# Kernel optimization log

Measured on AMD Instinct MI355X. Metric: run time of the kernel, lower is better.

## Reference

```python
import jax, jax.numpy as jnp
import numpy as np

B, S, D_MODEL, H = 4, 2048, 2048, 16
HD = D_MODEL // H  # 128
ROPE_BASE = 10000.0


def apply_rope(x):
    # x: [B, H, S, HD]; interleaved-pair rotary embedding along seq axis
    s, d = x.shape[2], x.shape[3]
    inv_freq = 1.0 / (ROPE_BASE ** (jnp.arange(0, d, 2, dtype=jnp.float32) / d))  # [d/2]
    ang = jnp.arange(s, dtype=jnp.float32)[:, None] * inv_freq[None, :]  # [S, d/2]
    cos, sin = jnp.cos(ang), jnp.sin(ang)
    x0, x1 = x[..., 0::2], x[..., 1::2]  # [B,H,S,d/2]
    o0 = x0 * cos - x1 * sin
    o1 = x0 * sin + x1 * cos
    return jnp.stack([o0, o1], axis=-1).reshape(x.shape)


def setup_inputs() -> dict:
    key = jax.random.key(0)
    ks = jax.random.split(key, 5)
    sc = 1.0 / np.sqrt(D_MODEL)
    return {
        "x": jax.random.normal(ks[0], (B, S, D_MODEL), dtype=jnp.float32),
        "Wq": jax.random.normal(ks[1], (D_MODEL, D_MODEL), dtype=jnp.float32) * sc,
        "Wk": jax.random.normal(ks[2], (D_MODEL, D_MODEL), dtype=jnp.float32) * sc,
        "Wv": jax.random.normal(ks[3], (D_MODEL, D_MODEL), dtype=jnp.float32) * sc,
        "Wo": jax.random.normal(ks[4], (D_MODEL, D_MODEL), dtype=jnp.float32) * sc,
        "bo": jnp.zeros((D_MODEL,), dtype=jnp.float32),
    }


def reference(x, Wq, Wk, Wv, Wo, bo):
    b, s, _ = x.shape
    # torch Linear: y = x @ W.T (no qkv bias)
    q = (x @ Wq.T).reshape(b, s, H, HD).transpose(0, 2, 1, 3)  # [B,H,S,HD]
    k = (x @ Wk.T).reshape(b, s, H, HD).transpose(0, 2, 1, 3)
    v = (x @ Wv.T).reshape(b, s, H, HD).transpose(0, 2, 1, 3)
    q = apply_rope(q)
    k = apply_rope(k)
    scores = jnp.einsum("bhqd,bhkd->bhqk", q, k)
    causal = jnp.tril(jnp.ones((s, s), dtype=bool))
    scores = jnp.where(causal, scores, -jnp.inf)
    attn = jax.nn.softmax(scores / jnp.sqrt(jnp.float32(HD)), axis=-1)
    # dropout p=0.0 -> identity
    ctx = jnp.einsum("bhqk,bhkd->bqhd", attn, v).reshape(b, s, H * HD)
    return ctx @ Wo.T + bo
```

## Files before the change

kernel.cpp:

```cpp
#include <hip/hip_runtime.h>
#include <hip/hip_bf16.h>
#include <math.h>

#define B_  4
#define S_  2048
#define DM  2048
#define H_  16
#define HD_ 128

typedef __bf16 bf16;
typedef __bf16 bf16x4 __attribute__((ext_vector_type(4)));
typedef __bf16 bf16x8 __attribute__((ext_vector_type(8)));
typedef float  f32x4  __attribute__((ext_vector_type(4)));

__device__ __forceinline__ void gload_lds16(const bf16* g, bf16* l) {
  __builtin_amdgcn_global_load_lds(
      (const __attribute__((address_space(1))) void*)g,
      (__attribute__((address_space(3))) void*)l, 16, 0, 0);
}

__global__ void cast_f32_bf16(const float* __restrict__ src, bf16* __restrict__ dst, int n4) {
  int stride = gridDim.x * blockDim.x;
  for (int i = blockIdx.x * blockDim.x + threadIdx.x; i < n4; i += stride) {
    float4 v = reinterpret_cast<const float4*>(src)[i];
    bf16x4 o = { (bf16)v.x, (bf16)v.y, (bf16)v.z, (bf16)v.w };
    reinterpret_cast<bf16x4*>(dst)[i] = o;
  }
}

__global__ void rope_table_k(float* __restrict__ tab) {
  int idx = blockIdx.x * blockDim.x + threadIdx.x;
  if (idx >= S_ * (HD_ / 2)) return;
  int pos = idx >> 6, i = idx & 63;
  float inv = powf(10000.0f, -(2.0f * i) / (float)HD_);
  float ang = (float)pos * inv;
  tab[2 * idx]     = cosf(ang);
  tab[2 * idx + 1] = sinf(ang);
}

template<int EPI>
__global__ __launch_bounds__(512, 2)
void gemm512(const bf16* __restrict__ A, const bf16* __restrict__ Bt,
             bf16* __restrict__ Oq, bf16* __restrict__ Ok, bf16* __restrict__ Ovt,
             float* __restrict__ Cf, const float* __restrict__ bias,
             const float* __restrict__ tab, int N, int K) {
  __shared__ bf16 lds[61440];
  const int tid = threadIdx.x;
  const int w = tid >> 6, l = tid & 63;
  const int lr = l & 15, lg = l >> 4;
  const int row0 = blockIdx.y * 512, col0 = blockIdx.x * 128;
  const int wm = w >> 1, wn = w & 1;
  const int NT = K / 32;

  auto stage = [&](int t, int c) {
    const bf16* Ab = A + (size_t)row0 * K + t * 32;
    const bf16* Bb = Bt + (size_t)col0 * K + t * 32;
    bf16* base = lds + c * 20480;
#pragma unroll
    for (int i = 0; i < 4; ++i) {
      int D = w * 4096 + i * 1024 + l * 16;
      int r = D >> 6;
      int gk = ((D & 63) ^ (((r >> 1) & 3) << 4)) >> 1;
      gload_lds16(Ab + (size_t)r * K + gk, base + ((w * 4096 + i * 1024) >> 1));
    }
    {
      int D = w * 1024 + l * 16;
      int r = D >> 6;
      int gk = ((D & 63) ^ (((r >> 1) & 3) << 4)) >> 1;
      gload_lds16(Bb + (size_t)r * K + gk, base + 16384 + ((w * 1024) >> 1));
    }
  };

  int offA[8], offB[4];
#pragma unroll
  for (int mi = 0; mi < 8; ++mi) {
    int r = wm * 128 + mi * 16 + lr;
    offA[mi] = r * 64 + ((lg * 16) ^ (((r >> 1) & 3) << 4));
  }
#pragma unroll
  for (int ni = 0; ni < 4; ++ni) {
    int r = wn * 64 + ni * 16 + lr;
    offB[ni] = 32768 + r * 64 + ((lg * 16) ^ (((r >> 1) & 3) << 4));
  }

  f32x4 acc[8][4] = {};
  stage(0, 0);
  stage(1, 1);

  for (int t = 0; t < NT; ++t) {
    const int c = t % 3;
    if (t + 2 < NT) {
      stage(t + 2, (t + 2) % 3);
      asm volatile("s_waitcnt vmcnt(10)" ::: "memory");
    } else if (t + 1 < NT) {
      asm volatile("s_waitcnt vmcnt(5)" ::: "memory");
    } else {
      asm volatile("s_waitcnt vmcnt(0)" ::: "memory");
    }
    __builtin_amdgcn_s_barrier();

    const char* bb = (const char*)lds + c * 40960;
    bf16x8 af[8], bfr[4];
#pragma unroll
    for (int mi = 0; mi < 8; ++mi) af[mi] = *reinterpret_cast<const bf16x8*>(bb + offA[mi]);
#pragma unroll
    for (int ni = 0; ni < 4; ++ni) bfr[ni] = *reinterpret_cast<const bf16x8*>(bb + offB[ni]);

    __builtin_amdgcn_s_setprio(1);
#pragma unroll
    for (int mi = 0; mi < 8; ++mi)
#pragma unroll
      for (int ni = 0; ni < 4; ++ni)
        acc[mi][ni] = __builtin_amdgcn_mfma_f32_16x16x32_bf16(af[mi], bfr[ni], acc[mi][ni], 0, 0, 0);
    __builtin_amdgcn_s_setprio(0);
    __builtin_amdgcn_s_barrier();
  }

#pragma unroll
  for (int mi = 0; mi < 8; ++mi) {
    int rb = row0 + wm * 128 + mi * 16 + lg * 4;
#pragma unroll
    for (int ni = 0; ni < 4; ++ni) {
      int gc = col0 + wn * 64 + ni * 16 + lr;
      if (EPI == 1) {
#pragma unroll
        for (int j = 0; j < 4; ++j)
          Cf[(size_t)(rb + j) * N + gc] = acc[mi][ni][j] + bias[gc];
      } else {
        int reg = col0 >> 11;
        int cc = gc & 2047;
        if (reg == 2) {
          int bb2 = rb >> 11, s = rb & 2047;
          int hh = cc >> 7, dd = cc & 127;
          bf16x4 pack = { (bf16)acc[mi][ni][0], (bf16)acc[mi][ni][1],
                          (bf16)acc[mi][ni][2], (bf16)acc[mi][ni][3] };
          *reinterpret_cast<bf16x4*>(Ovt + (((size_t)(bb2 * H_ + hh) * HD_ + dd) << 11) + s) = pack;
        } else {
          bf16* Dst = (reg == 0) ? Oq : Ok;
          float scale = (reg == 0) ? 0.08838834764831845f : 1.0f;
          int i2 = (cc & 127) >> 1;
          float sgn = (lr & 1) ? 1.0f : -1.0f;
#pragma unroll
          for (int j = 0; j < 4; ++j) {
            float own = acc[mi][ni][j];
            float par = __shfl_xor(own, 1);
            int s = (rb + j) & (S_ - 1);
            float2 cs = reinterpret_cast<const float2*>(tab)[s * 64 + i2];
            Dst[(size_t)(rb + j) * 2048 + cc] = (bf16)((own * cs.x + sgn * par * cs.y) * scale);
          }
        }
      }
    }
  }
}

__global__ __launch_bounds__(512, 4)
void attn_fwd(const bf16* __restrict__ Q, const bf16* __restrict__ K,
              const bf16* __restrict__ Vt, bf16* __restrict__ O) {
  __shared__ bf16 Ks[2][64 * 128];
  __shared__ bf16 Vs[2][128 * 64];
  __shared__ bf16 Ps[8][16 * 64];
  const int tid = threadIdx.x;
  const int w = tid >> 6, l = tid & 63;
  const int lr = l & 15, lg = l >> 4;
  const int bx = blockIdx.x;
  const int h = blockIdx.y, b = blockIdx.z;
  const size_t bbase = (size_t)b * S_ * DM + (size_t)h * HD_;
  const bf16* vtb = Vt + (size_t)(b * H_ + h) * HD_ * S_;

#pragma unroll 1
  for (int pass = 0; pass < 2; ++pass) {
    const int qt = pass ? bx : (15 - bx);
    const int q0 = qt * 128 + w * 16;
    const int ktmax = 2 * qt + 1;

    bf16x8 qf[4];
#pragma unroll
    for (int kb = 0; kb < 4; ++kb)
      qf[kb] = *reinterpret_cast<const bf16x8*>(Q + bbase + (size_t)(q0 + lr) * DM + kb * 32 + lg * 8);

    float m_r = -INFINITY;
    float l_r = 0.f;
    f32x4 o[8] = {};

#pragma unroll
    for (int i = 0; i < 2; ++i) {
      int X = w * 2048 + i * 1024 + l * 16;
      int r = X >> 8, scb = (X & 255) ^ ((r & 7) << 4);
      gload_lds16(K + bbase + (size_t)r * DM + (scb >> 1), &Ks[0][(w * 2048 + i * 1024) >> 1]);
    }
#pragma unroll
    for (int i = 0; i < 2; ++i) {
      int X = w * 2048 + i * 1024 + l * 16;
      int d = X >> 7, scb = (X & 127) ^ ((d & 7) << 4);
      gload_lds16(vtb + (size_t)d * S_ + (scb >> 1), &Vs[0][(w * 2048 + i * 1024) >> 1]);
    }

    for (int kt = 0; kt <= ktmax; ++kt) {
      const int buf = kt & 1;
      if (kt < ktmax) {
        const int nk = (kt + 1) * 64;
#pragma unroll
        for (int i = 0; i < 2; ++i) {
          int X = w * 2048 + i * 1024 + l * 16;
          int r = X >> 8, scb = (X & 255) ^ ((r & 7) << 4);
          gload_lds16(K + bbase + (size_t)(nk + r) * DM + (scb >> 1),
                      &Ks[buf ^ 1][(w * 2048 + i * 1024) >> 1]);
        }
#pragma unroll
        for (int i = 0; i < 2; ++i) {
          int X = w * 2048 + i * 1024 + l * 16;
          int d = X >> 7, scb = (X & 127) ^ ((d & 7) << 4);
          gload_lds16(vtb + (size_t)d * S_ + nk + (scb >> 1),
                      &Vs[buf ^ 1][(w * 2048 + i * 1024) >> 1]);
        }
        asm volatile("s_waitcnt vmcnt(4)" ::: "memory");
      } else {
        asm volatile("s_waitcnt vmcnt(0)" ::: "memory");
      }
      __builtin_amdgcn_s_barrier();

      f32x4 sc4[4];
      __builtin_amdgcn_s_setprio(1);
#pragma unroll
      for (int cb = 0; cb < 4; ++cb) {
        sc4[cb] = f32x4{0.f, 0.f, 0.f, 0.f};
        int r = cb * 16 + lr;
#pragma unroll
        for (int kb = 0; kb < 4; ++kb) {
          int off = r * 256 + ((kb * 64 + lg * 16) ^ ((lr & 7) << 4));
          bf16x8 kf = *reinterpret_cast<const bf16x8*>((const char*)Ks[buf] + off);
          sc4[cb] = __builtin_amdgcn_mfma_f32_16x16x32_bf16(kf, qf[kb], sc4[cb], 0, 0, 0);
        }
      }
      __builtin_amdgcn_s_setprio(0);

      const int kv0 = kt * 64;
      if (kv0 + 63 > q0) {
        const int qq = q0 + lr;
#pragma unroll
        for (int cb = 0; cb < 4; ++cb)
#pragma unroll
          for (int jj = 0; jj < 4; ++jj)
            if (kv0 + cb * 16 + lg * 4 + jj > qq) sc4[cb][jj] = -INFINITY;
      }

      float tm = -INFINITY;
#pragma unroll
      for (int cb = 0; cb < 4; ++cb)
#pragma unroll
        for (int jj = 0; jj < 4; ++jj) tm = fmaxf(tm, sc4[cb][jj]);
      tm = fmaxf(tm, __shfl_xor(tm, 16));
      tm = fmaxf(tm, __shfl_xor(tm, 32));
      float mnew = fmaxf(m_r, tm);
      float sc_f = __expf(m_r - mnew);
      m_r = mnew;
      float rs = 0.f;
#pragma unroll
      for (int cb = 0; cb < 4; ++cb)
#pragma unroll
        for (int jj = 0; jj < 4; ++jj) {
          float p = __expf(sc4[cb][jj] - mnew);
          sc4[cb][jj] = p;
          rs += p;
        }
      rs += __shfl_xor(rs, 16);
      rs += __shfl_xor(rs, 32);
      l_r = l_r * sc_f + rs;

      float scO[4];
#pragma unroll
      for (int j = 0; j < 4; ++j) scO[j] = __shfl(sc_f, lg * 4 + j);
#pragma unroll
      for (int nb = 0; nb < 8; ++nb)
#pragma unroll
        for (int j = 0; j < 4; ++j) o[nb][j] *= scO[j];

#pragma unroll
      for (int cb = 0; cb < 4; ++cb) {
        bf16x4 pk = { (bf16)sc4[cb][0], (bf16)sc4[cb][1], (bf16)sc4[cb][2], (bf16)sc4[cb][3] };
        int off = lr * 128 + ((cb * 32 + lg * 8) ^ ((lr & 7) << 4));
        *reinterpret_cast<bf16x4*>((char*)Ps[w] + off) = pk;
      }

      bf16x8 pf[2];
#pragma unroll
      for (int kc = 0; kc < 2; ++kc) {
        int off = lr * 128 + ((kc * 64 + lg * 16) ^ ((lr & 7) << 4));
        pf[kc] = *reinterpret_cast<const bf16x8*>((const char*)Ps[w] + off);
      }
      __builtin_amdgcn_s_setprio(1);
#pragma unroll
      for (int nb = 0; nb < 8; ++nb) {
        int d = nb * 16 + lr;
#pragma unroll
        for (int kc = 0; kc < 2; ++kc) {
          int off = d * 128 + ((kc * 64 + lg * 16) ^ ((lr & 7) << 4));
          bf16x8 vf = *reinterpret_cast<const bf16x8*>((const char*)Vs[buf] + off);
          o[nb] = __builtin_amdgcn_mfma_f32_16x16x32_bf16(pf[kc], vf, o[nb], 0, 0, 0);
        }
      }
      __builtin_amdgcn_s_setprio(0);

      asm volatile("s_waitcnt lgkmcnt(0)" ::: "memory");
      __builtin_amdgcn_s_barrier();
    }

    float lO[4];
#pragma unroll
    for (int j = 0; j < 4; ++j) lO[j] = __shfl(l_r, lg * 4 + j);
#pragma unroll
    for (int j = 0; j < 4; ++j) {
      float inv = 1.0f / lO[j];
      size_t rowoff = bbase + (size_t)(q0 + lg * 4 + j) * DM;
#pragma unroll
      for (int nb = 0; nb < 8; ++nb)
        O[rowoff + nb * 16 + lr] = (bf16)(o[nb][j] * inv);
    }
  }
}

extern "C" void kernel_launch(void* const* d_in, const int* in_sizes, int n_in,
                              void* d_out, int out_size, void* d_ws, size_t ws_size,
                              hipStream_t stream) {
  const float* x  = (const float*)d_in[0];
  const float* Wq = (const float*)d_in[1];
  const float* Wk = (const float*)d_in[2];
  const float* Wv = (const float*)d_in[3];
  const float* Wo = (const float*)d_in[4];
  const float* bo = (const float*)d_in[5];
  float* out = (float*)d_out;

  const size_t NX = (size_t)B_ * S_ * DM;
  const size_t NW = (size_t)DM * DM;
  char* ws = (char*)d_ws;
  bf16* xb   = (bf16*)ws; ws += NX * 2;
  bf16* wqkv = (bf16*)ws; ws += 3 * NW * 2;
  bf16* wob  = (bf16*)ws; ws += NW * 2;
  bf16* qb   = (bf16*)ws; ws += NX * 2;
  bf16* kb   = (bf16*)ws; ws += NX * 2;
  bf16* vt   = (bf16*)ws; ws += NX * 2;
  bf16* ctxb = (bf16*)ws; ws += NX * 2;
  float* tab = (float*)ws; ws += (size_t)S_ * 64 * 2 * sizeof(float);

  cast_f32_bf16<<<(int)((NX / 4 + 255) / 256), 256, 0, stream>>>(x, xb, (int)(NX / 4));
  cast_f32_bf16<<<(int)((NW / 4 + 255) / 256), 256, 0, stream>>>(Wq, wqkv, (int)(NW / 4));
  cast_f32_bf16<<<(int)((NW / 4 + 255) / 256), 256, 0, stream>>>(Wk, wqkv + NW, (int)(NW / 4));
  cast_f32_bf16<<<(int)((NW / 4 + 255) / 256), 256, 0, stream>>>(Wv, wqkv + 2 * NW, (int)(NW / 4));
  cast_f32_bf16<<<(int)((NW / 4 + 255) / 256), 256, 0, stream>>>(Wo, wob, (int)(NW / 4));
  rope_table_k<<<(S_ * 64 + 255) / 256, 256, 0, stream>>>(tab);

  const int M = B_ * S_;
  gemm512<0><<<dim3(3 * DM / 128, M / 512), 512, 0, stream>>>(
      xb, wqkv, qb, kb, vt, nullptr, nullptr, tab, 3 * DM, DM);

  attn_fwd<<<dim3(8, H_, B_), 512, 0, stream>>>(qb, kb, vt, ctxb);

  gemm512<1><<<dim3(DM / 128, M / 512), 512, 0, stream>>>(
      ctxb, wob, nullptr, nullptr, nullptr, out, bo, nullptr, DM, DM);
}
```

Before: 472.6 us.

## Rework projection GEMM into 256x256 tiles with quarter-step K pipeline

Replaces the 512x128 block tile, 3-stage K=32 pipeline with a 256x256 tile over a 2x4 wave grid. It uses a double-buffered K=64 stage split into two halves, with loads interleaved across four quarter-steps per iteration. The square tile cuts global traffic per FLOP and overlaps staging with MFMA work at finer granularity. In exchange it uses 128KB of LDS, which limits occupancy to one block per CU despite the launch bounds, and adds more barriers per iteration.

New measurement: 438.8 us. 1.08x faster.

```diff
diff --git a/kernel.cpp b/kernel.cpp
--- a/kernel.cpp
+++ b/kernel.cpp
@@ -40,100 +40,111 @@
 
 template<int EPI>
 __global__ __launch_bounds__(512, 2)
-void gemm512(const bf16* __restrict__ A, const bf16* __restrict__ Bt,
-             bf16* __restrict__ Oq, bf16* __restrict__ Ok, bf16* __restrict__ Ovt,
-             float* __restrict__ Cf, const float* __restrict__ bias,
-             const float* __restrict__ tab, int N, int K) {
-  __shared__ bf16 lds[61440];
+void gemm8p(const bf16* __restrict__ A, const bf16* __restrict__ Bt,
+            bf16* __restrict__ Oq, bf16* __restrict__ Ok, bf16* __restrict__ Ovt,
+            float* __restrict__ Cf, const float* __restrict__ bias,
+            const float* __restrict__ tab, int N, int K) {
+  __shared__ char lds[131072];
   const int tid = threadIdx.x;
   const int w = tid >> 6, l = tid & 63;
   const int lr = l & 15, lg = l >> 4;
-  const int row0 = blockIdx.y * 512, col0 = blockIdx.x * 128;
-  const int wm = w >> 1, wn = w & 1;
-  const int NT = K / 32;
-
-  auto stage = [&](int t, int c) {
-    const bf16* Ab = A + (size_t)row0 * K + t * 32;
-    const bf16* Bb = Bt + (size_t)col0 * K + t * 32;
-    bf16* base = lds + c * 20480;
-#pragma unroll
-    for (int i = 0; i < 4; ++i) {
-      int D = w * 4096 + i * 1024 + l * 16;
-      int r = D >> 6;
-      int gk = ((D & 63) ^ (((r >> 1) & 3) << 4)) >> 1;
-      gload_lds16(Ab + (size_t)r * K + gk, base + ((w * 4096 + i * 1024) >> 1));
-    }
-    {
-      int D = w * 1024 + l * 16;
-      int r = D >> 6;
-      int gk = ((D & 63) ^ (((r >> 1) & 3) << 4)) >> 1;
-      gload_lds16(Bb + (size_t)r * K + gk, base + 16384 + ((w * 1024) >> 1));
+  const int wm = w >> 2, wn = w & 3;
+  const int row0 = blockIdx.y * 256, col0 = blockIdx.x * 256;
+  const int NT = K >> 6;
+
+  auto stageSlot = [&](int isB, int kh, int kt2) {
+    const bf16* src = isB ? (Bt + (size_t)col0 * K) : (A + (size_t)row0 * K);
+    char* dstbase = (char*)lds + (kt2 & 1) * 65536 + isB * 32768 + kh * 16384;
+    const int kcol = kt2 * 64 + kh * 32;
+#pragma unroll
+    for (int u = 0; u < 2; ++u) {
+      int D = w * 2048 + u * 1024 + l * 16;
+      int r = D >> 6, cb = D & 63;
+      int sc = cb ^ (((r >> 1) & 3) << 4);
+      gload_lds16(src + (size_t)r * K + kcol + (sc >> 1),
+                  (bf16*)(dstbase + w * 2048 + u * 1024));
     }
   };
 
-  int offA[8], offB[4];
-#pragma unroll
-  for (int mi = 0; mi < 8; ++mi) {
-    int r = wm * 128 + mi * 16 + lr;
-    offA[mi] = r * 64 + ((lg * 16) ^ (((r >> 1) & 3) << 4));
-  }
+  const int swzt = ((lr >> 1) & 3) << 4;
+  int offA[2][4], offB[4];
+#pragma unroll
+  for (int qm = 0; qm < 2; ++qm)
+#pragma unroll
+    for (int mi = 0; mi < 4; ++mi) {
+      int r = wm * 128 + qm * 64 + mi * 16 + lr;
+      offA[qm][mi] = r * 64 + ((lg * 16) ^ swzt);
+    }
 #pragma unroll
   for (int ni = 0; ni < 4; ++ni) {
     int r = wn * 64 + ni * 16 + lr;
-    offB[ni] = 32768 + r * 64 + ((lg * 16) ^ (((r >> 1) & 3) << 4));
+    offB[ni] = 32768 + r * 64 + ((lg * 16) ^ swzt);
   }
 
   f32x4 acc[8][4] = {};
-  stage(0, 0);
-  stage(1, 1);
-
-  for (int t = 0; t < NT; ++t) {
-    const int c = t % 3;
-    if (t + 2 < NT) {
-      stage(t + 2, (t + 2) % 3);
-      asm volatile("s_waitcnt vmcnt(10)" ::: "memory");
-    } else if (t + 1 < NT) {
-      asm volatile("s_waitcnt vmcnt(5)" ::: "memory");
-    } else {
-      asm volatile("s_waitcnt vmcnt(0)" ::: "memory");
-    }
-    __builtin_amdgcn_s_barrier();
-
-    const char* bb = (const char*)lds + c * 40960;
-    bf16x8 af[8], bfr[4];
-#pragma unroll
-    for (int mi = 0; mi < 8; ++mi) af[mi] = *reinterpret_cast<const bf16x8*>(bb + offA[mi]);
-#pragma unroll
-    for (int ni = 0; ni < 4; ++ni) bfr[ni] = *reinterpret_cast<const bf16x8*>(bb + offB[ni]);
-
-    __builtin_amdgcn_s_setprio(1);
-#pragma unroll
-    for (int mi = 0; mi < 8; ++mi)
+
+  stageSlot(0, 0, 0); stageSlot(1, 0, 0);
+  stageSlot(0, 1, 0); stageSlot(1, 1, 0);
+  if (NT > 1) { stageSlot(0, 0, 1); stageSlot(1, 0, 1); }
+
+#pragma unroll 1
+  for (int kt = 0; kt < NT; ++kt) {
+    const char* bufb = (const char*)lds + (kt & 1) * 65536;
+#pragma unroll
+    for (int q = 0; q < 4; ++q) {
+      const int qm = q & 1 ? 1 : 0;
+      const int kh = q >> 1;
+      const int qmm = (q == 1 || q == 3) ? 1 : 0;
+      if (q == 0) {
+        if (kt + 1 < NT) asm volatile("s_waitcnt vmcnt(8)" ::: "memory");
+        else             asm volatile("s_waitcnt vmcnt(4)" ::: "memory");
+        __builtin_amdgcn_s_barrier();
+      } else if (q == 2) {
+        if (kt + 1 < NT) asm volatile("s_waitcnt vmcnt(8)" ::: "memory");
+        else             asm volatile("s_waitcnt vmcnt(0)" ::: "memory");
+        __builtin_amdgcn_s_barrier();
+      }
+      const char* bb = bufb + kh * 16384;
+      bf16x8 af[4], bfr[4];
+#pragma unroll
+      for (int mi = 0; mi < 4; ++mi)
+        af[mi] = *reinterpret_cast<const bf16x8*>(bb + offA[qmm][mi]);
 #pragma unroll
       for (int ni = 0; ni < 4; ++ni)
-        acc[mi][ni] = __builtin_amdgcn_mfma_f32_16x16x32_bf16(af[mi], bfr[ni], acc[mi][ni], 0, 0, 0);
-    __builtin_amdgcn_s_setprio(0);
-    __builtin_amdgcn_s_barrier();
-  }
-
-#pragma unroll
-  for (int mi = 0; mi < 8; ++mi) {
-    int rb = row0 + wm * 128 + mi * 16 + lg * 4;
+        bfr[ni] = *reinterpret_cast<const bf16x8*>(bb + offB[ni]);
+      if (q < 2) { if (kt + 1 < NT) stageSlot(q & 1, 1, kt + 1); }
+      else       { if (kt + 2 < NT) stageSlot(q & 1, 0, kt + 2); }
+      __builtin_amdgcn_s_barrier();
+      asm volatile("s_waitcnt lgkmcnt(0)" ::: "memory");
+      __builtin_amdgcn_s_setprio(1);
+#pragma unroll
+      for (int mi = 0; mi < 4; ++mi)
+#pragma unroll
+        for (int ni = 0; ni < 4; ++ni)
+          acc[qmm * 4 + mi][ni] =
+              __builtin_amdgcn_mfma_f32_16x16x32_bf16(af[mi], bfr[ni], acc[qmm * 4 + mi][ni], 0, 0, 0);
+      __builtin_amdgcn_s_setprio(0);
+    }
+  }
+
+#pragma unroll
+  for (int ai = 0; ai < 8; ++ai) {
+    int rb = row0 + wm * 128 + ai * 16 + lg * 4;
 #pragma unroll
     for (int ni = 0; ni < 4; ++ni) {
       int gc = col0 + wn * 64 + ni * 16 + lr;
       if (EPI == 1) {
 #pragma unroll
         for (int j = 0; j < 4; ++j)
-          Cf[(size_t)(rb + j) * N + gc] = acc[mi][ni][j] + bias[gc];
+          Cf[(size_t)(rb + j) * N + gc] = acc[ai][ni][j] + bias[gc];
       } else {
         int reg = col0 >> 11;
         int cc = gc & 2047;
         if (reg == 2) {
           int bb2 = rb >> 11, s = rb & 2047;
           int hh = cc >> 7, dd = cc & 127;
-          bf16x4 pack = { (bf16)acc[mi][ni][0], (bf16)acc[mi][ni][1],
-                          (bf16)acc[mi][ni][2], (bf16)acc[mi][ni][3] };
+          bf16x4 pack = { (bf16)acc[ai][ni][0], (bf16)acc[ai][ni][1],
+                          (bf16)acc[ai][ni][2], (bf16)acc[ai][ni][3] };
           *reinterpret_cast<bf16x4*>(Ovt + (((size_t)(bb2 * H_ + hh) * HD_ + dd) << 11) + s) = pack;
         } else {
           bf16* Dst = (reg == 0) ? Oq : Ok;
@@ -142,7 +153,7 @@
           float sgn = (lr & 1) ? 1.0f : -1.0f;
 #pragma unroll
           for (int j = 0; j < 4; ++j) {
-            float own = acc[mi][ni][j];
+            float own = acc[ai][ni][j];
             float par = __shfl_xor(own, 1);
             int s = (rb + j) & (S_ - 1);
             float2 cs = reinterpret_cast<const float2*>(tab)[s * 64 + i2];
@@ -351,11 +362,11 @@
   rope_table_k<<<(S_ * 64 + 255) / 256, 256, 0, stream>>>(tab);
 
   const int M = B_ * S_;
-  gemm512<0><<<dim3(3 * DM / 128, M / 512), 512, 0, stream>>>(
+  gemm8p<0><<<dim3(3 * DM / 256, M / 256), 512, 0, stream>>>(
       xb, wqkv, qb, kb, vt, nullptr, nullptr, tab, 3 * DM, DM);
 
   attn_fwd<<<dim3(8, H_, B_), 512, 0, stream>>>(qb, kb, vt, ctxb);
 
-  gemm512<1><<<dim3(DM / 128, M / 512), 512, 0, stream>>>(
+  gemm8p<1><<<dim3(DM / 256, M / 256), 512, 0, stream>>>(
       ctxb, wob, nullptr, nullptr, nullptr, out, bo, nullptr, DM, DM);
 }
```
